# Optimization experiments

Hardware: AMD Instinct MI355X
Metric: run time of the kernel (lower is better)

Reference implementation:

```python
import jax, jax.numpy as jnp
import numpy as np

B = 65536
D = 8          # model dim (hard-wired in source)
H = 2          # num_heads
A = 20         # act_size
L = 5          # tokens per embedding stream


def _attn_layer(x, Wqkv, bqkv, Wo, bo, Wl, bl):
    # x: [B, S, D]
    Bx, S, Dx = x.shape
    hd = Dx // H
    qkv = x @ Wqkv.T + bqkv                      # [B, S, 3D]
    q, k, v = jnp.split(qkv, 3, axis=-1)
    def split_heads(t):
        return t.reshape(Bx, S, H, hd).transpose(0, 2, 1, 3)  # [B,H,S,hd]
    q, k, v = split_heads(q), split_heads(k), split_heads(v)
    scores = jnp.einsum('bhqd,bhkd->bhqk', q, k) * (hd ** -0.5)
    attn = jax.nn.softmax(scores, axis=-1)       # dropout inactive at eval
    o = jnp.einsum('bhqk,bhkd->bhqd', attn, v)
    o = o.transpose(0, 2, 1, 3).reshape(Bx, S, Dx)
    x = x + (o @ Wo.T + bo)                      # residual after attention
    h = jax.nn.relu(x @ Wl.T + bl)               # linear + relu
    return x + h                                 # second residual


def setup_inputs() -> dict:
    key = jax.random.key(0)
    ks = jax.random.split(key, 20)
    s = 1.0 / np.sqrt(D)
    inp = {
        'dice_type': jax.random.randint(ks[0], (B, L), 0, 15),
        'dice_star': jax.random.randint(ks[1], (B, L), 0, 15),
        'summon_lvl': jax.random.randint(ks[2], (B, L), 0, 2),
        'emb_dice': jax.random.normal(ks[3], (15, D), jnp.float32),
        'emb_star': jax.random.normal(ks[4], (15, D), jnp.float32),
        'emb_btns': jax.random.normal(ks[5], (2, D), jnp.float32),
        'Wout': jax.random.normal(ks[6], (A, D), jnp.float32) * s,
        'bout': jnp.zeros((A,), jnp.float32),
    }
    for i in range(2):
        o = 7 + 5 * i
        inp[f'Wqkv{i}'] = jax.random.normal(ks[o], (3 * D, D), jnp.float32) * s
        inp[f'bqkv{i}'] = jnp.zeros((3 * D,), jnp.float32)
        inp[f'Wo{i}'] = jax.random.normal(ks[o + 1], (D, D), jnp.float32) * s
        inp[f'bo{i}'] = jnp.zeros((D,), jnp.float32)
        inp[f'Wl{i}'] = jax.random.normal(ks[o + 2], (D, D), jnp.float32) * s
        inp[f'bl{i}'] = jnp.zeros((D,), jnp.float32)
    return inp


def reference(dice_type, dice_star, summon_lvl,
              emb_dice, emb_star, emb_btns,
              Wqkv0, bqkv0, Wo0, bo0, Wl0, bl0,
              Wqkv1, bqkv1, Wo1, bo1, Wl1, bl1,
              Wout, bout):
    x = jnp.concatenate([emb_dice[dice_type],
                         emb_star[dice_star],
                         emb_btns[summon_lvl]], axis=1)  # [B, 15, D]
    x = _attn_layer(x, Wqkv0, bqkv0, Wo0, bo0, Wl0, bl0)
    x = _attn_layer(x, Wqkv1, bqkv1, Wo1, bo1, Wl1, bl1)
    x = jnp.mean(x, axis=1)                               # [B, D]
    return x @ Wout.T + bout                              # [B, A]
```

## Files before the change

kernel.cpp:

```cpp
#include <hip/hip_runtime.h>
#include <math.h>

#define EPB 16
#define BTOT 65536
#define C_SCALE 0.72134752044f

typedef _Float16 h2 __attribute__((ext_vector_type(2)));
typedef __fp16 fp16v2 __attribute__((ext_vector_type(2)));

#define WQKV1 0
#define BQKV1 96
#define WO0   108
#define BO0   140
#define WL0   144
#define BL0   176
#define WO1   180
#define BO1   212
#define WL1   216
#define BL1   248
#define WV1P  256
#define BV1F  288

__device__ __forceinline__ float exp2_fast(float x) { return __builtin_amdgcn_exp2f(x); }
__device__ __forceinline__ float rcp_fast(float x)  { return __builtin_amdgcn_rcpf(x); }
__device__ __forceinline__ h2 pkrtz(float a, float b) {
  fp16v2 r = __builtin_amdgcn_cvt_pkrtz(a, b);
  return __builtin_bit_cast(h2, r);
}
__device__ __forceinline__ float fdot2f(h2 a, h2 b, float c) {
#if defined(__has_builtin) && __has_builtin(__builtin_amdgcn_fdot2)
  return __builtin_amdgcn_fdot2(a, b, c, false);
#else
  return (float)a.x * (float)b.x + (float)a.y * (float)b.y + c;
#endif
}

union F4H2 { float4 f; h2 h[4]; };

__device__ __forceinline__ void mm8_h2(const h2* __restrict__ wp, int woff, int boff,
                                       const h2 in2[4], h2 out2[4])
{
#pragma unroll
  for (int c2 = 0; c2 < 4; ++c2) {
    h2 acc = wp[boff + c2];
#pragma unroll
    for (int p = 0; p < 4; ++p) {
      acc += (h2)(in2[p].x) * wp[woff + c2 * 8 + 2 * p];
      acc += (h2)(in2[p].y) * wp[woff + c2 * 8 + 2 * p + 1];
    }
    out2[c2] = acc;
  }
}

__global__ void BetterBot_setup(const float* __restrict__ Wqkv1, const float* __restrict__ bqkv1,
                                const float* __restrict__ Wo0, const float* __restrict__ bo0,
                                const float* __restrict__ Wl0, const float* __restrict__ bl0,
                                const float* __restrict__ Wo1, const float* __restrict__ bo1,
                                const float* __restrict__ Wl1, const float* __restrict__ bl1,
                                h2* __restrict__ ws)
{
  const int tid = threadIdx.x;
  if (tid < 96) {
    const int c2 = tid >> 3, j = tid & 7;
    int ra, rb; float s = 1.0f;
    if (c2 < 4)      { ra = 2 * c2; rb = ra + 1; s = C_SCALE; }
    else if (c2 < 8) { ra = 8 + 2 * (c2 - 4); rb = ra + 1; }
    else             { ra = 16 + (c2 - 8); rb = ra + 4; }
    ws[tid] = pkrtz(Wqkv1[ra * 8 + j] * s, Wqkv1[rb * 8 + j] * s);
  } else if (tid < 108) {
    const int c2 = tid - 96;
    int ra, rb; float s = 1.0f;
    if (c2 < 4)      { ra = 2 * c2; rb = ra + 1; s = C_SCALE; }
    else if (c2 < 8) { ra = 8 + 2 * (c2 - 4); rb = ra + 1; }
    else             { ra = 16 + (c2 - 8); rb = ra + 4; }
    ws[tid] = pkrtz(bqkv1[ra] * s, bqkv1[rb] * s);
  } else if (tid < 140) {
    const int k = tid - 108, c2 = k >> 3, j = k & 7, p = j >> 1;
    const int col = (j & 1) ? (p + 4) : p;
    ws[tid] = pkrtz(Wo0[(2 * c2) * 8 + col], Wo0[(2 * c2 + 1) * 8 + col]);
  } else if (tid < 144) {
    const int c2 = tid - 140;
    ws[tid] = pkrtz(bo0[2 * c2], bo0[2 * c2 + 1]);
  } else if (tid < 176) {
    const int k = tid - 144, c2 = k >> 3, j = k & 7;
    ws[tid] = pkrtz(Wl0[(2 * c2) * 8 + j], Wl0[(2 * c2 + 1) * 8 + j]);
  } else if (tid < 180) {
    const int c2 = tid - 176;
    ws[tid] = pkrtz(bl0[2 * c2], bl0[2 * c2 + 1]);
  } else if (tid < 212) {
    const int k = tid - 180, c2 = k >> 3, j = k & 7, p = j >> 1;
    const int col = (j & 1) ? (p + 4) : p;
    ws[tid] = pkrtz(Wo1[(2 * c2) * 8 + col], Wo1[(2 * c2 + 1) * 8 + col]);
  } else if (tid < 216) {
    const int c2 = tid - 212;
    ws[tid] = pkrtz(bo1[2 * c2], bo1[2 * c2 + 1]);
  } else if (tid < 248) {
    const int k = tid - 216, c2 = k >> 3, j = k & 7;
    ws[tid] = pkrtz(Wl1[(2 * c2) * 8 + j], Wl1[(2 * c2 + 1) * 8 + j]);
  } else if (tid < 252) {
    const int c2 = tid - 248;
    ws[tid] = pkrtz(bl1[2 * c2], bl1[2 * c2 + 1]);
  }
  if (tid < 32) {
    const int r = tid >> 2, p = tid & 3;
    const int row = 16 + (r >> 1) + (r & 1) * 4;
    ws[WV1P + tid] = pkrtz(Wqkv1[row * 8 + 2 * p], Wqkv1[row * 8 + 2 * p + 1]);
  } else if (tid < 40) {
    const int r = tid - 32;
    const int row = 16 + (r >> 1) + (r & 1) * 4;
    ((float*)(ws + BV1F))[r] = bqkv1[row];
  }
}

__global__ __launch_bounds__(256, 8) void BetterBot_44169443672375_kernel(
    const int* __restrict__ dice_type, const int* __restrict__ dice_star,
    const int* __restrict__ summon_lvl,
    const float* __restrict__ emb_dice, const float* __restrict__ emb_star,
    const float* __restrict__ emb_btns,
    const float* __restrict__ Wout, const float* __restrict__ bout,
    const float* __restrict__ Wqkv0, const float* __restrict__ bqkv0,
    const h2* __restrict__ wp,
    float* __restrict__ out)
{
  __shared__ __align__(16) h2 qT16[32][4];
  __shared__ __align__(16) h2 kT16[32][4];
  __shared__ __align__(16) h2 vT[32][4];
  __shared__ __align__(16) h2 xT[32][4];
  __shared__ h2 eT[32 * 33];
  __shared__ int idxT[EPB][16];
  __shared__ __align__(16) float kvb[EPB][15][12];

  const int tid = threadIdx.x;
  const int e = tid >> 4;
  const int t = tid & 15;
  const int ge = blockIdx.x * EPB + e;
  const float* wsf = (const float*)(wp + BV1F);

  int myc = 0;
  if (t < 15) {
    int c;
    if (t < 5)       c = dice_type[ge * 5 + t];
    else if (t < 10) c = 15 + dice_star[ge * 5 + (t - 5)];
    else             c = 30 + summon_lvl[ge * 5 + (t - 10)];
    idxT[e][t] = c;
    myc = c;
  }
  {
    const int c = tid >> 3;
    const int l8 = tid & 7;
    const float* er;
    if (c < 15)      er = emb_dice + 8 * c;
    else if (c < 30) er = emb_star + 8 * (c - 15);
    else             er = emb_btns + 8 * (c - 30);
    const float4 r0 = ((const float4*)er)[0];
    const float4 r1 = ((const float4*)er)[1];
    float r[8] = {r0.x, r0.y, r0.z, r0.w, r1.x, r1.y, r1.z, r1.w};
    if (l8 < 4) xT[c][l8] = pkrtz(r[2 * l8], r[2 * l8 + 1]);
    float aq = bqkv0[l8], ak = bqkv0[8 + l8], av = bqkv0[16 + l8];
#pragma unroll
    for (int j = 0; j < 8; ++j) {
      aq = fmaf(r[j], Wqkv0[l8 * 8 + j], aq);
      ak = fmaf(r[j], Wqkv0[(8 + l8) * 8 + j], ak);
      av = fmaf(r[j], Wqkv0[(16 + l8) * 8 + j], av);
    }
    aq *= C_SCALE;
    const float aq_p = __shfl_xor(aq, 1);
    const float ak_p = __shfl_xor(ak, 1);
    const float av_p = __shfl_xor(av, 4);
    if ((l8 & 1) == 0) {
      qT16[c][l8 >> 1] = pkrtz(aq, aq_p);
      kT16[c][l8 >> 1] = pkrtz(ak, ak_p);
    }
    if (l8 < 4) vT[c][l8] = pkrtz(av, av_p);
  }
  __syncthreads();

  {
    const int qi = tid >> 3;
    const int l8 = tid & 7;
    F4H2 qr; qr.f = *(const float4*)(&qT16[qi][0]);
#pragma unroll
    for (int jj = 0; jj < 4; ++jj) {
      const int ki = l8 + 8 * jj;
      F4H2 kr; kr.f = *(const float4*)(&kT16[ki][0]);
      const float s0 = fdot2f(qr.h[0], kr.h[0], fdot2f(qr.h[1], kr.h[1], 0.f));
      const float s1 = fdot2f(qr.h[2], kr.h[2], fdot2f(qr.h[3], kr.h[3], 0.f));
      eT[qi * 33 + ki] = pkrtz(exp2_fast(s0), exp2_fast(s1));
    }
  }
  __syncthreads();

  h2 x2[4] = {(h2)(_Float16)0.f, (h2)(_Float16)0.f, (h2)(_Float16)0.f, (h2)(_Float16)0.f};
  h2 q2[4];
  const h2 ONE0 = {(_Float16)1.f, (_Float16)0.f};
  const h2 ONE1 = {(_Float16)0.f, (_Float16)1.f};
  if (t < 15) {
    F4H2 xx; xx.f = *(const float4*)(&xT[myc][0]);
#pragma unroll
    for (int p = 0; p < 4; ++p) x2[p] = xx.h[p];

    h2 o2[4] = {(h2)(_Float16)0.f, (h2)(_Float16)0.f, (h2)(_Float16)0.f, (h2)(_Float16)0.f};
    float sum0 = 0.f, sum1 = 0.f;
    const h2* myE = eT + myc * 33;
#pragma unroll
    for (int u = 0; u < 15; ++u) {
      const int uc = idxT[e][u];
      const h2 ee2 = myE[uc];
      F4H2 vv; vv.f = *(const float4*)(&vT[uc][0]);
      sum0 = fdot2f(ee2, ONE0, sum0);
      sum1 = fdot2f(ee2, ONE1, sum1);
      o2[0] += ee2 * vv.h[0];
      o2[1] += ee2 * vv.h[1];
      o2[2] += ee2 * vv.h[2];
      o2[3] += ee2 * vv.h[3];
    }
    const h2 rp2 = pkrtz(rcp_fast(sum0), rcp_fast(sum1));
#pragma unroll
    for (int p = 0; p < 4; ++p) o2[p] *= rp2;

    h2 y2[4], xn2[4], hh2[4];
    mm8_h2(wp, WO0, BO0, o2, y2);
#pragma unroll
    for (int p = 0; p < 4; ++p) xn2[p] = x2[p] + y2[p];
    mm8_h2(wp, WL0, BL0, xn2, hh2);
    const h2 z2 = (h2)(_Float16)0.f;
#pragma unroll
    for (int p = 0; p < 4; ++p) x2[p] = xn2[p] + __builtin_elementwise_max(hh2[p], z2);

    h2 qkv2[8];
#pragma unroll
    for (int c2 = 0; c2 < 8; ++c2) {
      h2 acc = wp[BQKV1 + c2];
#pragma unroll
      for (int p = 0; p < 4; ++p) {
        acc += (h2)(x2[p].x) * wp[WQKV1 + c2 * 8 + 2 * p];
        acc += (h2)(x2[p].y) * wp[WQKV1 + c2 * 8 + 2 * p + 1];
      }
      qkv2[c2] = acc;
    }
#pragma unroll
    for (int p = 0; p < 4; ++p) q2[p] = qkv2[p];
    float vv[8];
#pragma unroll
    for (int r = 0; r < 8; ++r) {
      float acc = wsf[r];
#pragma unroll
      for (int p = 0; p < 4; ++p) acc = fdot2f(x2[p], wp[WV1P + r * 4 + p], acc);
      vv[r] = acc;
    }
    F4H2 ka;
#pragma unroll
    for (int p = 0; p < 4; ++p) ka.h[p] = qkv2[4 + p];
    *(float4*)(&kvb[e][t][0]) = ka.f;
    *(float4*)(&kvb[e][t][4]) = make_float4(vv[0], vv[1], vv[2], vv[3]);
    *(float4*)(&kvb[e][t][8]) = make_float4(vv[4], vv[5], vv[6], vv[7]);
  }
  __syncthreads();

  if (t < 15) {
    float o[8] = {0.f, 0.f, 0.f, 0.f, 0.f, 0.f, 0.f, 0.f};
    float sum0 = 0.f, sum1 = 0.f;
#pragma unroll
    for (int u = 0; u < 15; ++u) {
      F4H2 kk; kk.f = *(const float4*)(&kvb[e][u][0]);
      const float4 va = *(const float4*)(&kvb[e][u][4]);
      const float4 vb = *(const float4*)(&kvb[e][u][8]);
      const float s0 = fdot2f(q2[0], kk.h[0], fdot2f(q2[1], kk.h[1], 0.f));
      const float s1 = fdot2f(q2[2], kk.h[2], fdot2f(q2[3], kk.h[3], 0.f));
      const float e0 = exp2_fast(s0);
      const float e1 = exp2_fast(s1);
      sum0 += e0; sum1 += e1;
      o[0] = fmaf(e0, va.x, o[0]); o[1] = fmaf(e1, va.y, o[1]);
      o[2] = fmaf(e0, va.z, o[2]); o[3] = fmaf(e1, va.w, o[3]);
      o[4] = fmaf(e0, vb.x, o[4]); o[5] = fmaf(e1, vb.y, o[5]);
      o[6] = fmaf(e0, vb.z, o[6]); o[7] = fmaf(e1, vb.w, o[7]);
    }
    const float r0 = rcp_fast(sum0), r1 = rcp_fast(sum1);
    h2 po2[4];
#pragma unroll
    for (int i = 0; i < 4; ++i) po2[i] = pkrtz(o[2 * i] * r0, o[2 * i + 1] * r1);

    h2 y2[4], xn2[4], hh2[4];
    mm8_h2(wp, WO1, BO1, po2, y2);
#pragma unroll
    for (int p = 0; p < 4; ++p) xn2[p] = x2[p] + y2[p];
    mm8_h2(wp, WL1, BL1, xn2, hh2);
    const h2 z2 = (h2)(_Float16)0.f;
#pragma unroll
    for (int p = 0; p < 4; ++p) x2[p] = xn2[p] + __builtin_elementwise_max(hh2[p], z2);
  } else {
#pragma unroll
    for (int p = 0; p < 4; ++p) x2[p] = (h2)(_Float16)0.f;
  }

  float p[8];
#pragma unroll
  for (int i = 0; i < 4; ++i) { p[2 * i] = (float)x2[i].x; p[2 * i + 1] = (float)x2[i].y; }
#pragma unroll
  for (int j = 0; j < 8; ++j) p[j] += __shfl_xor(p[j], 1);
#pragma unroll
  for (int j = 0; j < 8; ++j) p[j] += __shfl_xor(p[j], 2);
#pragma unroll
  for (int j = 0; j < 8; ++j) p[j] += __shfl_xor(p[j], 4);
#pragma unroll
  for (int j = 0; j < 8; ++j) p[j] += __shfl_xor(p[j], 8);
  float mean[8];
#pragma unroll
  for (int j = 0; j < 8; ++j) mean[j] = p[j] * (1.0f / 15.0f);

  const int obase = ge * 20;
  {
    float acc = bout[t];
#pragma unroll
    for (int j = 0; j < 8; ++j) acc = fmaf(mean[j], Wout[t * 8 + j], acc);
    out[obase + t] = acc;
  }
  if (t < 4) {
    const int a = 16 + t;
    float acc = bout[a];
#pragma unroll
    for (int j = 0; j < 8; ++j) acc = fmaf(mean[j], Wout[a * 8 + j], acc);
    out[obase + a] = acc;
  }
}

extern "C" void kernel_launch(void* const* d_in, const int* in_sizes, int n_in,
                              void* d_out, int out_size, void* d_ws, size_t ws_size,
                              hipStream_t stream) {
  const int*   dice_type  = (const int*)d_in[0];
  const int*   dice_star  = (const int*)d_in[1];
  const int*   summon_lvl = (const int*)d_in[2];
  const float* emb_dice   = (const float*)d_in[3];
  const float* emb_star   = (const float*)d_in[4];
  const float* emb_btns   = (const float*)d_in[5];
  const float* Wout       = (const float*)d_in[6];
  const float* bout       = (const float*)d_in[7];
  const float* Wqkv0      = (const float*)d_in[8];
  const float* bqkv0      = (const float*)d_in[9];
  const float* Wo0        = (const float*)d_in[10];
  const float* bo0        = (const float*)d_in[11];
  const float* Wl0        = (const float*)d_in[12];
  const float* bl0        = (const float*)d_in[13];
  const float* Wqkv1      = (const float*)d_in[14];
  const float* bqkv1      = (const float*)d_in[15];
  const float* Wo1        = (const float*)d_in[16];
  const float* bo1        = (const float*)d_in[17];
  const float* Wl1        = (const float*)d_in[18];
  const float* bl1        = (const float*)d_in[19];
  float* out = (float*)d_out;
  h2* ws = (h2*)d_ws;

  hipLaunchKernelGGL(BetterBot_setup, dim3(1), dim3(256), 0, stream,
                     Wqkv1, bqkv1, Wo0, bo0, Wl0, bl0, Wo1, bo1, Wl1, bl1, ws);
  hipLaunchKernelGGL(BetterBot_44169443672375_kernel, dim3(BTOT / EPB), dim3(256), 0, stream,
                     dice_type, dice_star, summon_lvl,
                     emb_dice, emb_star, emb_btns, Wout, bout,
                     Wqkv0, bqkv0, (const h2*)ws, out);
}
```

Baseline: 126.9 us.

## Precompute layer-0 token tables once in setup kernel and copy into shared memory

Moves the per-block embedding projection, the layer-0 QK score exponentials and the V table into the single-block setup kernel, which writes them to workspace. Each main block now just copies a ~5KB table into LDS instead of recomputing it, which removes one barrier and the redundant ALU work in every block. The change also does the mean reduction with packed half shuffles, folds the 1/15 factor into a prescaled Wout, and sums the softmax denominators in fp16. These add precision risk from the fp16 accumulation and rely on the setup kernel's serial latency being small.

```diff
diff --git a/kernel.cpp b/kernel.cpp
--- a/kernel.cpp
+++ b/kernel.cpp
@@ -20,6 +20,16 @@
 #define BL1   248
 #define WV1P  256
 #define BV1F  288
+#define XT    304
+#define VT    432
+#define ET    560
+#define WOUTF 1616
+#define BOUTF 1776
+#define TBL0  304
+#define TBLV4 328
+#define XTO 0
+#define VTO 128
+#define ETO 256
 
 __device__ __forceinline__ float exp2_fast(float x) { return __builtin_amdgcn_exp2f(x); }
 __device__ __forceinline__ float rcp_fast(float x)  { return __builtin_amdgcn_rcpf(x); }
@@ -36,6 +46,7 @@
 }
 
 union F4H2 { float4 f; h2 h[4]; };
+union H2I { h2 h; int i; };
 
 __device__ __forceinline__ void mm8_h2(const h2* __restrict__ wp, int woff, int boff,
                                        const h2 in2[4], h2 out2[4])
@@ -52,14 +63,22 @@
   }
 }
 
-__global__ void BetterBot_setup(const float* __restrict__ Wqkv1, const float* __restrict__ bqkv1,
-                                const float* __restrict__ Wo0, const float* __restrict__ bo0,
-                                const float* __restrict__ Wl0, const float* __restrict__ bl0,
-                                const float* __restrict__ Wo1, const float* __restrict__ bo1,
-                                const float* __restrict__ Wl1, const float* __restrict__ bl1,
-                                h2* __restrict__ ws)
+__global__ void BetterBot_setup(
+    const float* __restrict__ emb_dice, const float* __restrict__ emb_star,
+    const float* __restrict__ emb_btns,
+    const float* __restrict__ Wout, const float* __restrict__ bout,
+    const float* __restrict__ Wqkv0, const float* __restrict__ bqkv0,
+    const float* __restrict__ Wqkv1, const float* __restrict__ bqkv1,
+    const float* __restrict__ Wo0, const float* __restrict__ bo0,
+    const float* __restrict__ Wl0, const float* __restrict__ bl0,
+    const float* __restrict__ Wo1, const float* __restrict__ bo1,
+    const float* __restrict__ Wl1, const float* __restrict__ bl1,
+    h2* __restrict__ ws)
 {
+  __shared__ float qs[32][8], ks[32][8], vs[32][8];
   const int tid = threadIdx.x;
+  float* wsf = (float*)ws;
+
   if (tid < 96) {
     const int c2 = tid >> 3, j = tid & 7;
     int ra, rb; float s = 1.0f;
@@ -108,25 +127,62 @@
   } else if (tid < 40) {
     const int r = tid - 32;
     const int row = 16 + (r >> 1) + (r & 1) * 4;
-    ((float*)(ws + BV1F))[r] = bqkv1[row];
+    wsf[BV1F + r] = bqkv1[row];
+  }
+  if (tid < 160)      wsf[WOUTF + tid] = Wout[tid] * (1.0f / 15.0f);
+  else if (tid < 180) wsf[BOUTF + tid - 160] = bout[tid - 160];
+
+  {
+    const int c = tid >> 3, l8 = tid & 7;
+    const float* er;
+    if (c < 15)      er = emb_dice + 8 * c;
+    else if (c < 30) er = emb_star + 8 * (c - 15);
+    else             er = emb_btns + 8 * (c - 30);
+    const float4 r0 = ((const float4*)er)[0];
+    const float4 r1 = ((const float4*)er)[1];
+    float r[8] = {r0.x, r0.y, r0.z, r0.w, r1.x, r1.y, r1.z, r1.w};
+    if (l8 < 4) ws[XT + c * 4 + l8] = pkrtz(r[2 * l8], r[2 * l8 + 1]);
+    float aq = bqkv0[l8], ak = bqkv0[8 + l8], av = bqkv0[16 + l8];
+#pragma unroll
+    for (int j = 0; j < 8; ++j) {
+      aq = fmaf(r[j], Wqkv0[l8 * 8 + j], aq);
+      ak = fmaf(r[j], Wqkv0[(8 + l8) * 8 + j], ak);
+      av = fmaf(r[j], Wqkv0[(16 + l8) * 8 + j], av);
+    }
+    qs[c][l8] = aq * C_SCALE;
+    ks[c][l8] = ak;
+    vs[c][l8] = av;
+  }
+  __syncthreads();
+
+  {
+    const int qi = tid >> 3, l8 = tid & 7;
+    float q[8];
+#pragma unroll
+    for (int j = 0; j < 8; ++j) q[j] = qs[qi][j];
+#pragma unroll
+    for (int jj = 0; jj < 4; ++jj) {
+      const int ki = l8 + 8 * jj;
+      float s0 = q[0] * ks[ki][0];
+      s0 = fmaf(q[1], ks[ki][1], s0); s0 = fmaf(q[2], ks[ki][2], s0); s0 = fmaf(q[3], ks[ki][3], s0);
+      float s1 = q[4] * ks[ki][4];
+      s1 = fmaf(q[5], ks[ki][5], s1); s1 = fmaf(q[6], ks[ki][6], s1); s1 = fmaf(q[7], ks[ki][7], s1);
+      ws[ET + qi * 33 + ki] = pkrtz(exp2_fast(s0), exp2_fast(s1));
+    }
+  }
+  if (tid < 32) {
+#pragma unroll
+    for (int p = 0; p < 4; ++p) ws[VT + tid * 4 + p] = pkrtz(vs[tid][p], vs[tid][p + 4]);
   }
 }
 
 __global__ __launch_bounds__(256, 8) void BetterBot_44169443672375_kernel(
     const int* __restrict__ dice_type, const int* __restrict__ dice_star,
     const int* __restrict__ summon_lvl,
-    const float* __restrict__ emb_dice, const float* __restrict__ emb_star,
-    const float* __restrict__ emb_btns,
-    const float* __restrict__ Wout, const float* __restrict__ bout,
-    const float* __restrict__ Wqkv0, const float* __restrict__ bqkv0,
     const h2* __restrict__ wp,
     float* __restrict__ out)
 {
-  __shared__ __align__(16) h2 qT16[32][4];
-  __shared__ __align__(16) h2 kT16[32][4];
-  __shared__ __align__(16) h2 vT[32][4];
-  __shared__ __align__(16) h2 xT[32][4];
-  __shared__ h2 eT[32 * 33];
+  __shared__ __align__(16) h2 tbl[1312];
   __shared__ int idxT[EPB][16];
   __shared__ __align__(16) float kvb[EPB][15][12];
 
@@ -134,8 +190,14 @@
   const int e = tid >> 4;
   const int t = tid & 15;
   const int ge = blockIdx.x * EPB + e;
-  const float* wsf = (const float*)(wp + BV1F);
-
+  const float* wsf = (const float*)wp;
+
+  {
+    float4* d = (float4*)tbl;
+    const float4* s = (const float4*)(wp + TBL0);
+    d[tid] = s[tid];
+    if (tid < TBLV4 - 256) d[256 + tid] = s[256 + tid];
+  }
   int myc = 0;
   if (t < 15) {
     int c;
@@ -145,76 +207,31 @@
     idxT[e][t] = c;
     myc = c;
   }
-  {
-    const int c = tid >> 3;
-    const int l8 = tid & 7;
-    const float* er;
-    if (c < 15)      er = emb_dice + 8 * c;
-    else if (c < 30) er = emb_star + 8 * (c - 15);
-    else             er = emb_btns + 8 * (c - 30);
-    const float4 r0 = ((const float4*)er)[0];
-    const float4 r1 = ((const float4*)er)[1];
-    float r[8] = {r0.x, r0.y, r0.z, r0.w, r1.x, r1.y, r1.z, r1.w};
-    if (l8 < 4) xT[c][l8] = pkrtz(r[2 * l8], r[2 * l8 + 1]);
-    float aq = bqkv0[l8], ak = bqkv0[8 + l8], av = bqkv0[16 + l8];
-#pragma unroll
-    for (int j = 0; j < 8; ++j) {
-      aq = fmaf(r[j], Wqkv0[l8 * 8 + j], aq);
-      ak = fmaf(r[j], Wqkv0[(8 + l8) * 8 + j], ak);
-      av = fmaf(r[j], Wqkv0[(16 + l8) * 8 + j], av);
-    }
-    aq *= C_SCALE;
-    const float aq_p = __shfl_xor(aq, 1);
-    const float ak_p = __shfl_xor(ak, 1);
-    const float av_p = __shfl_xor(av, 4);
-    if ((l8 & 1) == 0) {
-      qT16[c][l8 >> 1] = pkrtz(aq, aq_p);
-      kT16[c][l8 >> 1] = pkrtz(ak, ak_p);
-    }
-    if (l8 < 4) vT[c][l8] = pkrtz(av, av_p);
-  }
-  __syncthreads();
-
-  {
-    const int qi = tid >> 3;
-    const int l8 = tid & 7;
-    F4H2 qr; qr.f = *(const float4*)(&qT16[qi][0]);
-#pragma unroll
-    for (int jj = 0; jj < 4; ++jj) {
-      const int ki = l8 + 8 * jj;
-      F4H2 kr; kr.f = *(const float4*)(&kT16[ki][0]);
-      const float s0 = fdot2f(qr.h[0], kr.h[0], fdot2f(qr.h[1], kr.h[1], 0.f));
-      const float s1 = fdot2f(qr.h[2], kr.h[2], fdot2f(qr.h[3], kr.h[3], 0.f));
-      eT[qi * 33 + ki] = pkrtz(exp2_fast(s0), exp2_fast(s1));
-    }
-  }
   __syncthreads();
 
   h2 x2[4] = {(h2)(_Float16)0.f, (h2)(_Float16)0.f, (h2)(_Float16)0.f, (h2)(_Float16)0.f};
   h2 q2[4];
-  const h2 ONE0 = {(_Float16)1.f, (_Float16)0.f};
-  const h2 ONE1 = {(_Float16)0.f, (_Float16)1.f};
   if (t < 15) {
-    F4H2 xx; xx.f = *(const float4*)(&xT[myc][0]);
+    F4H2 xx; xx.f = *(const float4*)(&tbl[XTO + myc * 4]);
 #pragma unroll
     for (int p = 0; p < 4; ++p) x2[p] = xx.h[p];
 
     h2 o2[4] = {(h2)(_Float16)0.f, (h2)(_Float16)0.f, (h2)(_Float16)0.f, (h2)(_Float16)0.f};
-    float sum0 = 0.f, sum1 = 0.f;
-    const h2* myE = eT + myc * 33;
+    h2 os2 = (h2)(_Float16)0.f;
+    const h2* myE = tbl + ETO + myc * 33;
+    const int* myI = idxT[e];
 #pragma unroll
     for (int u = 0; u < 15; ++u) {
-      const int uc = idxT[e][u];
+      const int uc = myI[u];
       const h2 ee2 = myE[uc];
-      F4H2 vv; vv.f = *(const float4*)(&vT[uc][0]);
-      sum0 = fdot2f(ee2, ONE0, sum0);
-      sum1 = fdot2f(ee2, ONE1, sum1);
+      F4H2 vv; vv.f = *(const float4*)(&tbl[VTO + uc * 4]);
+      os2 += ee2;
       o2[0] += ee2 * vv.h[0];
       o2[1] += ee2 * vv.h[1];
       o2[2] += ee2 * vv.h[2];
       o2[3] += ee2 * vv.h[3];
     }
-    const h2 rp2 = pkrtz(rcp_fast(sum0), rcp_fast(sum1));
+    const h2 rp2 = pkrtz(rcp_fast((float)os2.x), rcp_fast((float)os2.y));
 #pragma unroll
     for (int p = 0; p < 4; ++p) o2[p] *= rp2;
 
@@ -243,7 +260,7 @@
     float vv[8];
 #pragma unroll
     for (int r = 0; r < 8; ++r) {
-      float acc = wsf[r];
+      float acc = wsf[BV1F + r];
 #pragma unroll
       for (int p = 0; p < 4; ++p) acc = fdot2f(x2[p], wp[WV1P + r * 4 + p], acc);
       vv[r] = acc;
@@ -293,33 +310,34 @@
     for (int p = 0; p < 4; ++p) x2[p] = (h2)(_Float16)0.f;
   }
 
-  float p[8];
-#pragma unroll
-  for (int i = 0; i < 4; ++i) { p[2 * i] = (float)x2[i].x; p[2 * i + 1] = (float)x2[i].y; }
-#pragma unroll
-  for (int j = 0; j < 8; ++j) p[j] += __shfl_xor(p[j], 1);
-#pragma unroll
-  for (int j = 0; j < 8; ++j) p[j] += __shfl_xor(p[j], 2);
-#pragma unroll
-  for (int j = 0; j < 8; ++j) p[j] += __shfl_xor(p[j], 4);
-#pragma unroll
-  for (int j = 0; j < 8; ++j) p[j] += __shfl_xor(p[j], 8);
-  float mean[8];
-#pragma unroll
-  for (int j = 0; j < 8; ++j) mean[j] = p[j] * (1.0f / 15.0f);
+  h2 p2[4];
+#pragma unroll
+  for (int p = 0; p < 4; ++p) p2[p] = x2[p];
+#pragma unroll
+  for (int m = 1; m <= 8; m <<= 1) {
+#pragma unroll
+    for (int p = 0; p < 4; ++p) {
+      H2I a; a.h = p2[p];
+      H2I b; b.i = __shfl_xor(a.i, m);
+      p2[p] += b.h;
+    }
+  }
+  float sx[8];
+#pragma unroll
+  for (int i = 0; i < 4; ++i) { sx[2 * i] = (float)p2[i].x; sx[2 * i + 1] = (float)p2[i].y; }
 
   const int obase = ge * 20;
   {
-    float acc = bout[t];
-#pragma unroll
-    for (int j = 0; j < 8; ++j) acc = fmaf(mean[j], Wout[t * 8 + j], acc);
+    float acc = wsf[BOUTF + t];
+#pragma unroll
+    for (int j = 0; j < 8; ++j) acc = fmaf(sx[j], wsf[WOUTF + t * 8 + j], acc);
     out[obase + t] = acc;
   }
   if (t < 4) {
     const int a = 16 + t;
-    float acc = bout[a];
-#pragma unroll
-    for (int j = 0; j < 8; ++j) acc = fmaf(mean[j], Wout[a * 8 + j], acc);
+    float acc = wsf[BOUTF + a];
+#pragma unroll
+    for (int j = 0; j < 8; ++j) acc = fmaf(sx[j], wsf[WOUTF + a * 8 + j], acc);
     out[obase + a] = acc;
   }
 }
@@ -351,9 +369,9 @@
   h2* ws = (h2*)d_ws;
 
   hipLaunchKernelGGL(BetterBot_setup, dim3(1), dim3(256), 0, stream,
-                     Wqkv1, bqkv1, Wo0, bo0, Wl0, bl0, Wo1, bo1, Wl1, bl1, ws);
+                     emb_dice, emb_star, emb_btns, Wout, bout,
+                     Wqkv0, bqkv0, Wqkv1, bqkv1,
+                     Wo0, bo0, Wl0, bl0, Wo1, bo1, Wl1, bl1, ws);
   hipLaunchKernelGGL(BetterBot_44169443672375_kernel, dim3(BTOT / EPB), dim3(256), 0, stream,
-                     dice_type, dice_star, summon_lvl,
-                     emb_dice, emb_star, emb_btns, Wout, bout,
-                     Wqkv0, bqkv0, (const h2*)ws, out);
-}
+                     dice_type, dice_star, summon_lvl, (const h2*)ws, out);
+}
```

New measurement: 123.2 us. 1.03x faster.
